# Kernel tuning notes

Measured on AMD Instinct MI355X. Metric: run time of the kernel, lower is better.

The kernel has to match this reference:

```python
import jax, jax.numpy as jnp
import numpy as np

N = 20000      # nodes (human PPI network scale)
E = 640000     # edges (avg degree 32)
PE, GOS, PROT = 128, 128, 480
OM_DIMS = [3, 3, 24, 24]          # transcriptome, proteome, effectome, interactome
D = 384                           # latent_space_dimension = 128 * 3 (jk 'cat')
H = 128                           # hidden_channels per layer
NEG_SLOPE = 0.1


def setup_inputs() -> dict:
    key = jax.random.key(0)
    ks = jax.random.split(key, 64)
    rn = lambda k, shp, s=0.05: jax.random.normal(k, shp, jnp.float32) * s
    inp = {
        "x": jax.random.normal(ks[0], (N, PE + GOS + PROT), jnp.float32),
        "x_ft": jax.random.normal(ks[1], (N, sum(OM_DIMS)), jnp.float32),
        "edge_index": jax.random.randint(ks[2], (2, E), 0, N),
    }
    i = 3
    def lin(fin, fout, name):
        nonlocal i
        inp["W_" + name] = rn(ks[i], (fin, fout)); inp["b_" + name] = jnp.zeros((fout,), jnp.float32)
        i += 1
    lin(PE, D, "pe"); lin(GOS, D, "gos"); lin(PROT, D, "prot")
    for j, d in enumerate(OM_DIMS):
        lin(d, D, f"om{j}")
    dims = [D, H, H, H]
    for j in range(3):
        lin(dims[j], dims[j + 1], f"c{j}")   # feature-branch GCN convs
        lin(dims[j], dims[j + 1], f"o{j}")   # omics-branch GCN convs
    lin(2 * D, D, "lat")
    lin(D, H, "drug"); lin(D, H, "dis")
    lin(H, 2, "odrug"); lin(H, 2, "odis")
    return inp


def _gcn(x, W, b, src, dst, deg_inv):
    # GCNConv(improved=True): A_hat = A + 2I, sym norm D^-1/2 A_hat D^-1/2
    h = x @ W                                  # [N, F_out]
    coef = deg_inv[src] * deg_inv[dst]         # [E]
    agg = jax.ops.segment_sum(h[src] * coef[:, None], dst, num_segments=N)
    agg = agg + h * (2.0 * deg_inv * deg_inv)[:, None]   # self loops (weight 2)
    return agg + b


def reference(x, x_ft, edge_index,
              W_pe, b_pe, W_gos, b_gos, W_prot, b_prot,
              W_om0, b_om0, W_om1, b_om1, W_om2, b_om2, W_om3, b_om3,
              W_c0, b_c0, W_o0, b_o0, W_c1, b_c1, W_o1, b_o1, W_c2, b_c2, W_o2, b_o2,
              W_lat, b_lat, W_drug, b_drug, W_dis, b_dis,
              W_odrug, b_odrug, W_odis, b_odis):
    act = lambda t: jax.nn.leaky_relu(t, NEG_SLOPE)
    src, dst = edge_index[0], edge_index[1]
    deg = jax.ops.segment_sum(jnp.ones((E,), jnp.float32), dst, num_segments=N) + 2.0
    deg_inv = jax.lax.rsqrt(deg)

    # encoders (features branch): pe | gosemsim | prot_emb slices of x
    pe = x[:, :PE]; gos = x[:, PE:PE + GOS]; prot = x[:, PE + GOS:PE + GOS + PROT]
    h = act(pe @ W_pe + b_pe + gos @ W_gos + b_gos + prot @ W_prot + b_prot)

    # encoders (omics branch): 3|3|24|24 slices of x_ft
    offs = np.cumsum([0] + OM_DIMS)
    Wom = [W_om0, W_om1, W_om2, W_om3]; bom = [b_om0, b_om1, b_om2, b_om3]
    g = act(sum(x_ft[:, offs[j]:offs[j + 1]] @ Wom[j] + bom[j] for j in range(4)))

    Wc = [W_c0, W_c1, W_c2]; bc = [b_c0, b_c1, b_c2]
    Wo = [W_o0, W_o1, W_o2]; bo = [b_o0, b_o1, b_o2]
    hs, gs = [], []
    for j in range(3):
        h = act(_gcn(h, Wc[j], bc[j], src, dst, deg_inv)); hs.append(h)
        g = act(_gcn(g, Wo[j], bo[j], src, dst, deg_inv)); gs.append(g)
    jk = jnp.concatenate(hs, axis=-1)          # [N, 384]
    jk_om = jnp.concatenate(gs, axis=-1)       # [N, 384]

    z = act(jnp.concatenate([jk, jk_om], axis=-1) @ W_lat + b_lat)  # [N, 384]
    drug = act(z @ W_drug + b_drug) @ W_odrug + b_odrug             # [N, 2]
    dis = act(z @ W_dis + b_dis) @ W_odis + b_odis                  # [N, 2]
    return jnp.concatenate([drug, dis], axis=-1)                    # [N, 4]
```

## Files before the change

### kernel.cpp

```cpp
#include <hip/hip_runtime.h>
#include <cstdint>

#define NN 20000
#define NNP 20096
#define NE 640000
#define NEG_SLOPE 0.1f
#define NSCAN 79
#define NSL 8
#define NPSL 2500
#define FBPS 160

typedef unsigned short ushort_t;
typedef __attribute__((ext_vector_type(8))) short short8;
typedef __attribute__((ext_vector_type(4))) float f32x4;
typedef __attribute__((ext_vector_type(2))) float f32x2;

__device__ __forceinline__ unsigned short f2bf(float f) {
    union { float f; unsigned u; } v; v.f = f;
    unsigned r = v.u + 0x7fffu + ((v.u >> 16) & 1u);
    return (unsigned short)(r >> 16);
}
__device__ __forceinline__ float bflo(unsigned u) { return __uint_as_float(u << 16); }
__device__ __forceinline__ float bfhi(unsigned u) { return __uint_as_float(u & 0xffff0000u); }

__device__ __forceinline__ int swz(int r) { return (r ^ (r >> 2)) & 3; }

__device__ __forceinline__ void gld_lds16(const void* g, void* l) {
    __builtin_amdgcn_global_load_lds(
        (const __attribute__((address_space(1))) void*)g,
        (__attribute__((address_space(3))) void*)l,
        16, 0, 0);
}

#define O_CAT   0
#define O_OM    282624
#define O_C0    307200
#define O_O0    356352
#define O_C1    405504
#define O_O1    421888
#define O_C2    438272
#define O_O2    454656
#define O_LAT   471040
#define O_HEADS 765952
#define WT_TOTAL 864256

__global__ __launch_bounds__(256) void pack_weights(
    const float* __restrict__ Wpe, const float* __restrict__ Wgos, const float* __restrict__ Wprot,
    const float* __restrict__ bpe, const float* __restrict__ bgos, const float* __restrict__ bprot,
    const float* __restrict__ Wom0, const float* __restrict__ Wom1,
    const float* __restrict__ Wom2, const float* __restrict__ Wom3,
    const float* __restrict__ bom0, const float* __restrict__ bom1,
    const float* __restrict__ bom2, const float* __restrict__ bom3,
    const float* __restrict__ Wc0, const float* __restrict__ Wo0,
    const float* __restrict__ Wc1, const float* __restrict__ Wo1,
    const float* __restrict__ Wc2, const float* __restrict__ Wo2,
    const float* __restrict__ Wlat,
    const float* __restrict__ Wdrug, const float* __restrict__ Wdis,
    const float* __restrict__ bdrug, const float* __restrict__ bdis,
    ushort_t* __restrict__ Wt, float* __restrict__ bcat, float* __restrict__ bomc,
    float* __restrict__ bheads)
{
    int i = blockIdx.x * blockDim.x + threadIdx.x;
    if (i < 282624) {
        int m = i / 736, k = i % 736;
        float v = (k < 128) ? Wpe[k * 384 + m]
                : (k < 256) ? Wgos[(k - 128) * 384 + m]
                            : Wprot[(k - 256) * 384 + m];
        Wt[O_CAT + i] = f2bf(v);
        return;
    }
    i -= 282624;
    if (i < 24576) {
        int m = i / 64, k = i % 64;
        float v = (k < 3)  ? Wom0[k * 384 + m]
                : (k < 6)  ? Wom1[(k - 3) * 384 + m]
                : (k < 30) ? Wom2[(k - 6) * 384 + m]
                : (k < 54) ? Wom3[(k - 30) * 384 + m] : 0.f;
        Wt[O_OM + i] = f2bf(v);
        return;
    }
    i -= 24576;
    if (i < 49152) { int m = i / 384, k = i % 384; Wt[O_C0 + i] = f2bf(Wc0[k * 128 + m]); return; }
    i -= 49152;
    if (i < 49152) { int m = i / 384, k = i % 384; Wt[O_O0 + i] = f2bf(Wo0[k * 128 + m]); return; }
    i -= 49152;
    if (i < 16384) { int m = i / 128, k = i % 128; Wt[O_C1 + i] = f2bf(Wc1[k * 128 + m]); return; }
    i -= 16384;
    if (i < 16384) { int m = i / 128, k = i % 128; Wt[O_O1 + i] = f2bf(Wo1[k * 128 + m]); return; }
    i -= 16384;
    if (i < 16384) { int m = i / 128, k = i % 128; Wt[O_C2 + i] = f2bf(Wc2[k * 128 + m]); return; }
    i -= 16384;
    if (i < 16384) { int m = i / 128, k = i % 128; Wt[O_O2 + i] = f2bf(Wo2[k * 128 + m]); return; }
    i -= 16384;
    if (i < 294912) { int m = i / 768, k = i % 768; Wt[O_LAT + i] = f2bf(Wlat[k * 384 + m]); return; }
    i -= 294912;
    if (i < 98304) {
        int m = i / 384, k = i % 384;
        float v = (m < 128) ? Wdrug[k * 128 + m] : Wdis[k * 128 + (m - 128)];
        Wt[O_HEADS + i] = f2bf(v);
        return;
    }
    i -= 98304;
    if (i < 384) { bcat[i] = bpe[i] + bgos[i] + bprot[i]; return; }
    i -= 384;
    if (i < 384) { bomc[i] = bom0[i] + bom1[i] + bom2[i] + bom3[i]; return; }
    i -= 384;
    if (i < 256) { bheads[i] = (i < 128) ? bdrug[i] : bdis[i - 128]; return; }
}

#define CVT_T1 (NN * 736 / 4)
__global__ __launch_bounds__(256) void convert_inputs(
    const float* __restrict__ x, const float* __restrict__ xft,
    ushort_t* __restrict__ xb, ushort_t* __restrict__ xftb)
{
    int i = blockIdx.x * blockDim.x + threadIdx.x;
    if (i < CVT_T1) {
        int base = i * 4;
        float4 v = *reinterpret_cast<const float4*>(&x[base]);
        unsigned long long p = (unsigned long long)f2bf(v.x)
                             | ((unsigned long long)f2bf(v.y) << 16)
                             | ((unsigned long long)f2bf(v.z) << 32)
                             | ((unsigned long long)f2bf(v.w) << 48);
        *reinterpret_cast<unsigned long long*>(&xb[base]) = p;
        return;
    }
    i -= CVT_T1;
    if (i < NN * 64) {
        int r = i >> 6, c = i & 63;
        float v = (c < 54) ? xft[r * 54 + c] : 0.f;
        xftb[i] = f2bf(v);
    }
}

__global__ __launch_bounds__(256) void count_deg_sliced(const int* __restrict__ dst, int* __restrict__ cnt)
{
    const int slice = blockIdx.x & (NSL - 1);
    const int blk = blockIdx.x >> 3;
    const int lo = slice * NPSL, hi = lo + NPSL;
    for (int e = blk * 256 + threadIdx.x; e < NE; e += FBPS * 256) {
        int d = dst[e];
        if (d >= lo && d < hi) atomicAdd(&cnt[d], 1);
    }
}

__global__ __launch_bounds__(256) void scan_blocksums(const int* __restrict__ cnt, int* __restrict__ bsum,
                                                      float* __restrict__ deg_inv)
{
    __shared__ int s[256];
    int t = threadIdx.x, i = blockIdx.x * 256 + t;
    int v = (i < NN) ? cnt[i] : 0;
    if (i < NN) deg_inv[i] = rsqrtf((float)v + 2.0f);
    s[t] = v;
    __syncthreads();
    for (int off = 128; off; off >>= 1) {
        if (t < off) s[t] += s[t + off];
        __syncthreads();
    }
    if (t == 0) bsum[blockIdx.x] = s[0];
}

__global__ __launch_bounds__(128) void scan_tops(const int* __restrict__ bsum,
                                                 int* __restrict__ boff, int* __restrict__ ofs)
{
    __shared__ int s[NSCAN];
    int t = threadIdx.x;
    if (t < NSCAN) s[t] = bsum[t];
    __syncthreads();
    if (t == 0) {
        int run = 0;
        for (int b = 0; b < NSCAN; b++) { int x = s[b]; s[b] = run; run += x; }
        ofs[NN] = run;
    }
    __syncthreads();
    if (t < NSCAN) boff[t] = s[t];
}

__global__ __launch_bounds__(256) void scan_apply(const int* __restrict__ cnt, const int* __restrict__ boff,
                                                  int* __restrict__ ofs, int* __restrict__ cursor)
{
    __shared__ int s[256];
    int t = threadIdx.x, i = blockIdx.x * 256 + t;
    int v = (i < NN) ? cnt[i] : 0;
    s[t] = v;
    __syncthreads();
    for (int off = 1; off < 256; off <<= 1) {
        int u = (t >= off) ? s[t - off] : 0;
        __syncthreads();
        s[t] += u;
        __syncthreads();
    }
    int excl = s[t] - v + boff[blockIdx.x];
    if (i < NN) { ofs[i] = excl; cursor[i] = excl; }
}

__global__ __launch_bounds__(256) void fill_csr_sliced(
    const int* __restrict__ src, const int* __restrict__ dst,
    const float* __restrict__ deg_inv, int* __restrict__ cursor,
    uint2* __restrict__ csr_pk)
{
    const int slice = blockIdx.x & (NSL - 1);
    const int blk = blockIdx.x >> 3;
    const int lo = slice * NPSL, hi = lo + NPSL;
    for (int e = blk * 256 + threadIdx.x; e < NE; e += FBPS * 256) {
        int d = dst[e];
        if (d >= lo && d < hi) {
            int s = src[e];
            int p = atomicAdd(&cursor[d], 1);
            float cf = deg_inv[s] * deg_inv[d];
            csr_pk[p] = make_uint2((unsigned)s * 256u, __float_as_uint(cf));
        }
    }
}

template<int BN, bool BIASACT, bool OUT_BF16>
__device__ __forceinline__ void gemm_body(
    ushort_t* As, ushort_t* Bs,
    const ushort_t* __restrict__ A, int lda,
    const ushort_t* __restrict__ Wt,
    const float* __restrict__ bias,
    float* __restrict__ Cf, ushort_t* __restrict__ Cb, int ldc,
    int nrows, int K, int row0, int col0)
{
    constexpr int BK = 32;
    constexpr int NI = (BN == 128) ? 4 : 2;

    const int t = threadIdx.x;
    const int w = t >> 6, lane = t & 63;
    const int wr = w >> 1, wc = w & 1;
    const int m16 = lane & 15, quad = lane >> 4;
    const int sr = lane >> 2;
    const int pgrp = lane & 3;

    f32x4 acc[4][NI];
#pragma unroll
    for (int mi = 0; mi < 4; mi++)
#pragma unroll
        for (int ni = 0; ni < NI; ni++) acc[mi][ni] = (f32x4)0.f;

    for (int k0 = 0; k0 < K; k0 += BK) {
#pragma unroll
        for (int p = 0; p < 2; p++) {
            int c = p * 4 + w;
            int r = c * 16 + sr;
            int q = pgrp ^ swz(r);
            gld_lds16(&A[(size_t)(row0 + r) * lda + k0 + q * 8], &As[c * 512]);
        }
#pragma unroll
        for (int p = 0; p < BN / 64; p++) {
            int c = p * 4 + w;
            int r = c * 16 + sr;
            int q = pgrp ^ swz(r);
            gld_lds16(&Wt[(size_t)(col0 + r) * K + k0 + q * 8], &Bs[c * 512]);
        }
        __syncthreads();

        short8 af[4], bfr[NI];
#pragma unroll
        for (int mi = 0; mi < 4; mi++) {
            int r = wr * 64 + mi * 16 + m16;
            int p = quad ^ swz(r);
            af[mi] = *reinterpret_cast<const short8*>(&As[r * 32 + p * 8]);
        }
#pragma unroll
        for (int ni = 0; ni < NI; ni++) {
            int n = wc * (NI * 16) + ni * 16 + m16;
            int p = quad ^ swz(n);
            bfr[ni] = *reinterpret_cast<const short8*>(&Bs[n * 32 + p * 8]);
        }
#pragma unroll
        for (int mi = 0; mi < 4; mi++)
#pragma unroll
            for (int ni = 0; ni < NI; ni++)
                acc[mi][ni] = __builtin_amdgcn_mfma_f32_16x16x32_bf16(af[mi], bfr[ni], acc[mi][ni], 0, 0, 0);
        __syncthreads();
    }

#pragma unroll
    for (int mi = 0; mi < 4; mi++) {
#pragma unroll
        for (int reg = 0; reg < 4; reg++) {
            int grow = row0 + wr * 64 + mi * 16 + quad * 4 + reg;
            if (grow >= nrows) continue;
#pragma unroll
            for (int ni = 0; ni < NI; ni++) {
                int gcol = col0 + wc * (NI * 16) + ni * 16 + m16;
                float v = acc[mi][ni][reg];
                if constexpr (BIASACT) {
                    v += bias[gcol];
                    v = (v > 0.f) ? v : NEG_SLOPE * v;
                }
                if constexpr (OUT_BF16) Cb[(size_t)grow * ldc + gcol] = f2bf(v);
                else                    Cf[(size_t)grow * ldc + gcol] = v;
            }
        }
    }
}

template<int BN, bool BIASACT, bool OUT_BF16>
__global__ __launch_bounds__(256) void mfma_gemm(
    const ushort_t* __restrict__ A, int lda,
    const ushort_t* __restrict__ Wt,
    const float* __restrict__ bias,
    float* __restrict__ Cf, ushort_t* __restrict__ Cb, int ldc,
    int nrows, int K)
{
    __shared__ ushort_t As[128 * 32];
    __shared__ ushort_t Bs[BN * 32];
    gemm_body<BN, BIASACT, OUT_BF16>(As, Bs, A, lda, Wt, bias, Cf, Cb, ldc, nrows, K,
                                     blockIdx.y * 128, blockIdx.x * BN);
}

__global__ __launch_bounds__(256) void mfma_gemm_dual(
    const ushort_t* __restrict__ A0, const ushort_t* __restrict__ A1, int lda,
    const ushort_t* __restrict__ W0, const ushort_t* __restrict__ W1,
    ushort_t* __restrict__ C0, ushort_t* __restrict__ C1, int ldc,
    int nrows, int K)
{
    __shared__ ushort_t As[128 * 32];
    __shared__ ushort_t Bs[64 * 32];
    const ushort_t* A  = blockIdx.z ? A1 : A0;
    const ushort_t* Wt = blockIdx.z ? W1 : W0;
    ushort_t*       Cb = blockIdx.z ? C1 : C0;
    gemm_body<64, false, true>(As, Bs, A, lda, Wt, nullptr, nullptr, Cb, ldc, nrows, K,
                               blockIdx.y * 128, blockIdx.x * 64);
}

__global__ __launch_bounds__(256) void aggregate_wave(
    const ushort_t* __restrict__ tabA, const ushort_t* __restrict__ tabB,
    const float* __restrict__ bc, const float* __restrict__ bo,
    const int* __restrict__ ofs, const uint2* __restrict__ csr_pk,
    const float* __restrict__ deg_inv,
    ushort_t* __restrict__ outb, int hcol, int gcol)
{
    __shared__ uint2 s_pk[4][64];
    const int w = threadIdx.x >> 6, lane = threadIdx.x & 63;
    const int task = blockIdx.x * 4 + w;
    const int slice = task / NN;
    const int i = task - slice * NN;
    const int chain = slice >> 1, half = slice & 1;
    const char* __restrict__ tabc = (const char*)(chain ? tabB : tabA);
    const float* __restrict__ bias = chain ? bo : bc;
    const int el = lane >> 3;
    const int fq = lane & 7;
    const unsigned lbyte = (unsigned)(half * 128 + fq * 16);

    const int start = ofs[i], end = ofs[i + 1];
    float acc[8];
#pragma unroll
    for (int q = 0; q < 8; q++) acc[q] = 0.f;

    for (int base = start; base < end; base += 64) {
        int n = end - base; if (n > 64) n = 64;
        if (lane < n) s_pk[w][lane] = csr_pk[base + lane];
        int j = el;
        for (; j + 8 < n; j += 16) {
            uint2 e0 = s_pk[w][j];
            uint2 e1 = s_pk[w][j + 8];
            uint4 p0 = *reinterpret_cast<const uint4*>(tabc + (e0.x + lbyte));
            uint4 p1 = *reinterpret_cast<const uint4*>(tabc + (e1.x + lbyte));
            float c0 = __uint_as_float(e0.y), c1 = __uint_as_float(e1.y);
            acc[0] = fmaf(bflo(p0.x), c0, acc[0]); acc[1] = fmaf(bfhi(p0.x), c0, acc[1]);
            acc[2] = fmaf(bflo(p0.y), c0, acc[2]); acc[3] = fmaf(bfhi(p0.y), c0, acc[3]);
            acc[4] = fmaf(bflo(p0.z), c0, acc[4]); acc[5] = fmaf(bfhi(p0.z), c0, acc[5]);
            acc[6] = fmaf(bflo(p0.w), c0, acc[6]); acc[7] = fmaf(bfhi(p0.w), c0, acc[7]);
            acc[0] = fmaf(bflo(p1.x), c1, acc[0]); acc[1] = fmaf(bfhi(p1.x), c1, acc[1]);
            acc[2] = fmaf(bflo(p1.y), c1, acc[2]); acc[3] = fmaf(bfhi(p1.y), c1, acc[3]);
            acc[4] = fmaf(bflo(p1.z), c1, acc[4]); acc[5] = fmaf(bfhi(p1.z), c1, acc[5]);
            acc[6] = fmaf(bflo(p1.w), c1, acc[6]); acc[7] = fmaf(bfhi(p1.w), c1, acc[7]);
        }
        if (j < n) {
            uint2 e0 = s_pk[w][j];
            uint4 p0 = *reinterpret_cast<const uint4*>(tabc + (e0.x + lbyte));
            float c0 = __uint_as_float(e0.y);
            acc[0] = fmaf(bflo(p0.x), c0, acc[0]); acc[1] = fmaf(bfhi(p0.x), c0, acc[1]);
            acc[2] = fmaf(bflo(p0.y), c0, acc[2]); acc[3] = fmaf(bfhi(p0.y), c0, acc[3]);
            acc[4] = fmaf(bflo(p0.z), c0, acc[4]); acc[5] = fmaf(bfhi(p0.z), c0, acc[5]);
            acc[6] = fmaf(bflo(p0.w), c0, acc[6]); acc[7] = fmaf(bfhi(p0.w), c0, acc[7]);
        }
    }
#pragma unroll
    for (int m = 8; m <= 32; m <<= 1) {
#pragma unroll
        for (int q = 0; q < 8; q++) acc[q] += __shfl_xor(acc[q], m);
    }
    if (el == 0) {
        float di = deg_inv[i];
        float c = 2.f * di * di;
        uint4 pv = *reinterpret_cast<const uint4*>(tabc + ((unsigned)i * 256u + lbyte));
        float sv[8] = {bflo(pv.x), bfhi(pv.x), bflo(pv.y), bfhi(pv.y),
                       bflo(pv.z), bfhi(pv.z), bflo(pv.w), bfhi(pv.w)};
        const int coloff = half * 64 + fq * 8;
        uint4 o;
        unsigned* op = &o.x;
#pragma unroll
        for (int q = 0; q < 8; q += 2) {
            float v0 = fmaf(sv[q],     c, acc[q])     + bias[coloff + q];
            float v1 = fmaf(sv[q + 1], c, acc[q + 1]) + bias[coloff + q + 1];
            v0 = (v0 > 0.f) ? v0 : NEG_SLOPE * v0;
            v1 = (v1 > 0.f) ? v1 : NEG_SLOPE * v1;
            op[q >> 1] = (unsigned)f2bf(v0) | ((unsigned)f2bf(v1) << 16);
        }
        int col = (chain ? gcol : hcol) + coloff;
        *reinterpret_cast<uint4*>(&outb[(size_t)i * 768 + col]) = o;
    }
}

__global__ __launch_bounds__(256) void heads_kernel(
    const float* __restrict__ tmpH,
    const float* __restrict__ Wod, const float* __restrict__ bod,
    const float* __restrict__ Wos, const float* __restrict__ bos,
    float* __restrict__ out)
{
    int w = threadIdx.x >> 6, lane = threadIdx.x & 63;
    int i = blockIdx.x * 4 + w;
    if (i >= NN) return;
    float a0 = 0.f, a1 = 0.f, d0 = 0.f, d1 = 0.f;
#pragma unroll
    for (int p = 0; p < 2; p++) {
        int k = lane + p * 64;
        float vd = tmpH[(size_t)i * 256 + k];
        float vs = tmpH[(size_t)i * 256 + 128 + k];
        a0 = fmaf(vd, Wod[k * 2 + 0], a0);
        a1 = fmaf(vd, Wod[k * 2 + 1], a1);
        d0 = fmaf(vs, Wos[k * 2 + 0], d0);
        d1 = fmaf(vs, Wos[k * 2 + 1], d1);
    }
    for (int off = 32; off; off >>= 1) {
        a0 += __shfl_down(a0, off);
        a1 += __shfl_down(a1, off);
        d0 += __shfl_down(d0, off);
        d1 += __shfl_down(d1, off);
    }
    if (lane == 0) {
        out[(size_t)i * 4 + 0] = a0 + bod[0];
        out[(size_t)i * 4 + 1] = a1 + bod[1];
        out[(size_t)i * 4 + 2] = d0 + bos[0];
        out[(size_t)i * 4 + 3] = d1 + bos[1];
    }
}

extern "C" void kernel_launch(void* const* d_in, const int* in_sizes, int n_in,
                              void* d_out, int out_size, void* d_ws, size_t ws_size,
                              hipStream_t stream)
{
    const float* x      = (const float*)d_in[0];
    const float* x_ft   = (const float*)d_in[1];
    const int*   eidx   = (const int*)d_in[2];
    const float* W_pe   = (const float*)d_in[3];
    const float* b_pe   = (const float*)d_in[4];
    const float* W_gos  = (const float*)d_in[5];
    const float* b_gos  = (const float*)d_in[6];
    const float* W_prot = (const float*)d_in[7];
    const float* b_prot = (const float*)d_in[8];
    const float* W_om0  = (const float*)d_in[9];
    const float* b_om0  = (const float*)d_in[10];
    const float* W_om1  = (const float*)d_in[11];
    const float* b_om1  = (const float*)d_in[12];
    const float* W_om2  = (const float*)d_in[13];
    const float* b_om2  = (const float*)d_in[14];
    const float* W_om3  = (const float*)d_in[15];
    const float* b_om3  = (const float*)d_in[16];
    const float* W_c[3] = {(const float*)d_in[17], (const float*)d_in[21], (const float*)d_in[25]};
    const float* b_c[3] = {(const float*)d_in[18], (const float*)d_in[22], (const float*)d_in[26]};
    const float* W_o[3] = {(const float*)d_in[19], (const float*)d_in[23], (const float*)d_in[27]};
    const float* b_o[3] = {(const float*)d_in[20], (const float*)d_in[24], (const float*)d_in[28]};
    const float* W_lat  = (const float*)d_in[29];
    const float* b_lat  = (const float*)d_in[30];
    const float* W_drug = (const float*)d_in[31];
    const float* b_drug = (const float*)d_in[32];
    const float* W_dis  = (const float*)d_in[33];
    const float* b_dis  = (const float*)d_in[34];
    const float* W_odrug= (const float*)d_in[35];
    const float* b_odrug= (const float*)d_in[36];
    const float* W_odis = (const float*)d_in[37];
    const float* b_odis = (const float*)d_in[38];
    float* out = (float*)d_out;

    const int* e_src = eidx;
    const int* e_dst = eidx + NE;

    char* p = (char*)d_ws;
    auto alloc = [&](size_t bytes) -> void* {
        void* r = (void*)p;
        p += (bytes + 255) & ~(size_t)255;
        return r;
    };
    ushort_t* Wt    = (ushort_t*)alloc((size_t)WT_TOTAL * 2);
    float* bcat     = (float*)alloc(384 * 4);
    float* bomc     = (float*)alloc(384 * 4);
    float* bheads   = (float*)alloc(256 * 4);
    float* deg_inv  = (float*)alloc((size_t)NN * 4);
    int*   cnt      = (int*)alloc((size_t)NN * 4);
    int*   ofs      = (int*)alloc((size_t)(NN + 1) * 4);
    int*   cursor   = (int*)alloc((size_t)NN * 4);
    int*   bsum     = (int*)alloc((size_t)NSCAN * 4);
    int*   boff     = (int*)alloc((size_t)NSCAN * 4);
    uint2* csr_pk   = (uint2*)alloc((size_t)NE * 8);
    ushort_t* xb    = (ushort_t*)alloc((size_t)NNP * 736 * 2);
    ushort_t* xftb  = (ushort_t*)alloc((size_t)NNP * 64 * 2);
    ushort_t* h0b   = (ushort_t*)alloc((size_t)NNP * 384 * 2);
    ushort_t* g0b   = (ushort_t*)alloc((size_t)NNP * 384 * 2);
    ushort_t* jkb   = (ushort_t*)alloc((size_t)NNP * 768 * 2);
    ushort_t* zb    = (ushort_t*)alloc((size_t)NNP * 384 * 2);
    ushort_t* tmpAb = (ushort_t*)alloc((size_t)NNP * 128 * 2);
    ushort_t* tmpBb = (ushort_t*)alloc((size_t)NNP * 128 * 2);
    float* tmpH     = (float*)alloc((size_t)NNP * 256 * 4);
    (void)ws_size; (void)in_sizes; (void)n_in; (void)out_size;

    {
        int total = WT_TOTAL + 384 + 384 + 256;
        pack_weights<<<dim3((total + 255) / 256), dim3(256), 0, stream>>>(
            W_pe, W_gos, W_prot, b_pe, b_gos, b_prot,
            W_om0, W_om1, W_om2, W_om3, b_om0, b_om1, b_om2, b_om3,
            W_c[0], W_o[0], W_c[1], W_o[1], W_c[2], W_o[2],
            W_lat, W_drug, W_dis, b_drug, b_dis, Wt, bcat, bomc, bheads);
    }
    convert_inputs<<<dim3((CVT_T1 + NN * 64 + 255) / 256), dim3(256), 0, stream>>>(x, x_ft, xb, xftb);

    hipMemsetAsync(cnt, 0, (size_t)NN * 4, stream);
    count_deg_sliced<<<dim3(NSL * FBPS), dim3(256), 0, stream>>>(e_dst, cnt);
    scan_blocksums<<<dim3(NSCAN), dim3(256), 0, stream>>>(cnt, bsum, deg_inv);
    scan_tops<<<dim3(1), dim3(128), 0, stream>>>(bsum, boff, ofs);
    scan_apply<<<dim3(NSCAN), dim3(256), 0, stream>>>(cnt, boff, ofs, cursor);
    fill_csr_sliced<<<dim3(NSL * FBPS), dim3(256), 0, stream>>>(e_src, e_dst, deg_inv, cursor, csr_pk);

    mfma_gemm<128, true, true><<<dim3(3, 157), dim3(256), 0, stream>>>(
        xb, 736, Wt + O_CAT, bcat, nullptr, h0b, 384, NN, 736);
    mfma_gemm<128, true, true><<<dim3(3, 157), dim3(256), 0, stream>>>(
        xftb, 64, Wt + O_OM, bomc, nullptr, g0b, 384, NN, 64);

    mfma_gemm_dual<<<dim3(2, 157, 2), dim3(256), 0, stream>>>(
        h0b, g0b, 384, Wt + O_C0, Wt + O_O0, tmpAb, tmpBb, 128, NN, 384);
    aggregate_wave<<<dim3(NN), dim3(256), 0, stream>>>(
        tmpAb, tmpBb, b_c[0], b_o[0], ofs, csr_pk, deg_inv, jkb, 0, 384);

    mfma_gemm_dual<<<dim3(2, 157, 2), dim3(256), 0, stream>>>(
        jkb + 0, jkb + 384, 768, Wt + O_C1, Wt + O_O1, tmpAb, tmpBb, 128, NN, 128);
    aggregate_wave<<<dim3(NN), dim3(256), 0, stream>>>(
        tmpAb, tmpBb, b_c[1], b_o[1], ofs, csr_pk, deg_inv, jkb, 128, 512);

    mfma_gemm_dual<<<dim3(2, 157, 2), dim3(256), 0, stream>>>(
        jkb + 128, jkb + 512, 768, Wt + O_C2, Wt + O_O2, tmpAb, tmpBb, 128, NN, 128);
    aggregate_wave<<<dim3(NN), dim3(256), 0, stream>>>(
        tmpAb, tmpBb, b_c[2], b_o[2], ofs, csr_pk, deg_inv, jkb, 256, 640);

    mfma_gemm<128, true, true><<<dim3(3, 157), dim3(256), 0, stream>>>(
        jkb, 768, Wt + O_LAT, b_lat, nullptr, zb, 384, NN, 768);

    mfma_gemm<128, true, false><<<dim3(2, 157), dim3(256), 0, stream>>>(
        zb, 384, Wt + O_HEADS, bheads, tmpH, nullptr, 256, NN, 384);
    heads_kernel<<<dim3((NN + 3) / 4), dim3(256), 0, stream>>>(
        tmpH, W_odrug, b_odrug, W_odis, b_odis, out);
}
```

Before: 499.8 us.

## Process both GCN chains per wave in fused aggregation, reading CSR directly

The aggregation kernel previously gave each wave one node-chain-half slice: 8 lanes per edge each loaded 16 bytes, and the 8 partial sums were then combined with shuffles. Now each wave handles one node across both chains and all 128 columns. 32 lanes cover the full 256-byte rows of both tables, and two edge groups are reduced with a single shuffle. This cuts repeated CSR reads and loop overhead fourfold and removes the LDS staging and the three-step shuffle reduction. In exchange, CSR entries are read directly from global memory by many lanes, and each wave has less edge-level parallelism.

```diff
diff --git a/kernel.cpp b/kernel.cpp
--- a/kernel.cpp
+++ b/kernel.cpp
@@ -325,71 +325,66 @@
                                blockIdx.y * 128, blockIdx.x * 64);
 }
 
-__global__ __launch_bounds__(256) void aggregate_wave(
+__global__ __launch_bounds__(256) void aggregate_fused(
     const ushort_t* __restrict__ tabA, const ushort_t* __restrict__ tabB,
     const float* __restrict__ bc, const float* __restrict__ bo,
     const int* __restrict__ ofs, const uint2* __restrict__ csr_pk,
     const float* __restrict__ deg_inv,
     ushort_t* __restrict__ outb, int hcol, int gcol)
 {
-    __shared__ uint2 s_pk[4][64];
     const int w = threadIdx.x >> 6, lane = threadIdx.x & 63;
-    const int task = blockIdx.x * 4 + w;
-    const int slice = task / NN;
-    const int i = task - slice * NN;
-    const int chain = slice >> 1, half = slice & 1;
-    const char* __restrict__ tabc = (const char*)(chain ? tabB : tabA);
-    const float* __restrict__ bias = chain ? bo : bc;
-    const int el = lane >> 3;
-    const int fq = lane & 7;
-    const unsigned lbyte = (unsigned)(half * 128 + fq * 16);
+    const int i = blockIdx.x * 4 + w;
+    const int el = lane >> 5;
+    const int fq = lane & 31;
+    const int chain = fq >> 4;
+    const unsigned lbyte = (unsigned)((fq & 15) * 16);
+    const char* __restrict__ tb = (const char*)(chain ? tabB : tabA);
 
     const int start = ofs[i], end = ofs[i + 1];
+    const float di = deg_inv[i];
+    const uint4 pv = *reinterpret_cast<const uint4*>(tb + ((unsigned)i * 256u + lbyte));
+
     float acc[8];
 #pragma unroll
     for (int q = 0; q < 8; q++) acc[q] = 0.f;
 
-    for (int base = start; base < end; base += 64) {
-        int n = end - base; if (n > 64) n = 64;
-        if (lane < n) s_pk[w][lane] = csr_pk[base + lane];
-        int j = el;
-        for (; j + 8 < n; j += 16) {
-            uint2 e0 = s_pk[w][j];
-            uint2 e1 = s_pk[w][j + 8];
-            uint4 p0 = *reinterpret_cast<const uint4*>(tabc + (e0.x + lbyte));
-            uint4 p1 = *reinterpret_cast<const uint4*>(tabc + (e1.x + lbyte));
-            float c0 = __uint_as_float(e0.y), c1 = __uint_as_float(e1.y);
-            acc[0] = fmaf(bflo(p0.x), c0, acc[0]); acc[1] = fmaf(bfhi(p0.x), c0, acc[1]);
-            acc[2] = fmaf(bflo(p0.y), c0, acc[2]); acc[3] = fmaf(bfhi(p0.y), c0, acc[3]);
-            acc[4] = fmaf(bflo(p0.z), c0, acc[4]); acc[5] = fmaf(bfhi(p0.z), c0, acc[5]);
-            acc[6] = fmaf(bflo(p0.w), c0, acc[6]); acc[7] = fmaf(bfhi(p0.w), c0, acc[7]);
-            acc[0] = fmaf(bflo(p1.x), c1, acc[0]); acc[1] = fmaf(bfhi(p1.x), c1, acc[1]);
-            acc[2] = fmaf(bflo(p1.y), c1, acc[2]); acc[3] = fmaf(bfhi(p1.y), c1, acc[3]);
-            acc[4] = fmaf(bflo(p1.z), c1, acc[4]); acc[5] = fmaf(bfhi(p1.z), c1, acc[5]);
-            acc[6] = fmaf(bflo(p1.w), c1, acc[6]); acc[7] = fmaf(bfhi(p1.w), c1, acc[7]);
-        }
-        if (j < n) {
-            uint2 e0 = s_pk[w][j];
-            uint4 p0 = *reinterpret_cast<const uint4*>(tabc + (e0.x + lbyte));
-            float c0 = __uint_as_float(e0.y);
-            acc[0] = fmaf(bflo(p0.x), c0, acc[0]); acc[1] = fmaf(bfhi(p0.x), c0, acc[1]);
-            acc[2] = fmaf(bflo(p0.y), c0, acc[2]); acc[3] = fmaf(bfhi(p0.y), c0, acc[3]);
-            acc[4] = fmaf(bflo(p0.z), c0, acc[4]); acc[5] = fmaf(bfhi(p0.z), c0, acc[5]);
-            acc[6] = fmaf(bflo(p0.w), c0, acc[6]); acc[7] = fmaf(bfhi(p0.w), c0, acc[7]);
-        }
-    }
-#pragma unroll
-    for (int m = 8; m <= 32; m <<= 1) {
-#pragma unroll
-        for (int q = 0; q < 8; q++) acc[q] += __shfl_xor(acc[q], m);
-    }
+#define FMA8(P, C) \
+    acc[0] = fmaf(bflo(P.x), C, acc[0]); acc[1] = fmaf(bfhi(P.x), C, acc[1]); \
+    acc[2] = fmaf(bflo(P.y), C, acc[2]); acc[3] = fmaf(bfhi(P.y), C, acc[3]); \
+    acc[4] = fmaf(bflo(P.z), C, acc[4]); acc[5] = fmaf(bfhi(P.z), C, acc[5]); \
+    acc[6] = fmaf(bflo(P.w), C, acc[6]); acc[7] = fmaf(bfhi(P.w), C, acc[7])
+
+    int j = start + el;
+    for (; j + 6 < end; j += 8) {
+        uint2 e0 = csr_pk[j];
+        uint2 e1 = csr_pk[j + 2];
+        uint2 e2 = csr_pk[j + 4];
+        uint2 e3 = csr_pk[j + 6];
+        uint4 p0 = *reinterpret_cast<const uint4*>(tb + (e0.x + lbyte));
+        uint4 p1 = *reinterpret_cast<const uint4*>(tb + (e1.x + lbyte));
+        uint4 p2 = *reinterpret_cast<const uint4*>(tb + (e2.x + lbyte));
+        uint4 p3 = *reinterpret_cast<const uint4*>(tb + (e3.x + lbyte));
+        float c0 = __uint_as_float(e0.y), c1 = __uint_as_float(e1.y);
+        float c2 = __uint_as_float(e2.y), c3 = __uint_as_float(e3.y);
+        FMA8(p0, c0); FMA8(p1, c1); FMA8(p2, c2); FMA8(p3, c3);
+    }
+    for (; j < end; j += 2) {
+        uint2 e0 = csr_pk[j];
+        uint4 p0 = *reinterpret_cast<const uint4*>(tb + (e0.x + lbyte));
+        float c0 = __uint_as_float(e0.y);
+        FMA8(p0, c0);
+    }
+#undef FMA8
+
+#pragma unroll
+    for (int q = 0; q < 8; q++) acc[q] += __shfl_xor(acc[q], 32);
+
     if (el == 0) {
-        float di = deg_inv[i];
-        float c = 2.f * di * di;
-        uint4 pv = *reinterpret_cast<const uint4*>(tabc + ((unsigned)i * 256u + lbyte));
+        const float* __restrict__ bias = chain ? bo : bc;
+        const int coloff = (fq & 15) * 8;
+        const float c = 2.f * di * di;
         float sv[8] = {bflo(pv.x), bfhi(pv.x), bflo(pv.y), bfhi(pv.y),
                        bflo(pv.z), bfhi(pv.z), bflo(pv.w), bfhi(pv.w)};
-        const int coloff = half * 64 + fq * 8;
         uint4 o;
         unsigned* op = &o.x;
 #pragma unroll
@@ -400,7 +395,7 @@
             v1 = (v1 > 0.f) ? v1 : NEG_SLOPE * v1;
             op[q >> 1] = (unsigned)f2bf(v0) | ((unsigned)f2bf(v1) << 16);
         }
-        int col = (chain ? gcol : hcol) + coloff;
+        const int col = (chain ? gcol : hcol) + coloff;
         *reinterpret_cast<uint4*>(&outb[(size_t)i * 768 + col]) = o;
     }
 }
@@ -531,17 +526,17 @@
 
     mfma_gemm_dual<<<dim3(2, 157, 2), dim3(256), 0, stream>>>(
         h0b, g0b, 384, Wt + O_C0, Wt + O_O0, tmpAb, tmpBb, 128, NN, 384);
-    aggregate_wave<<<dim3(NN), dim3(256), 0, stream>>>(
+    aggregate_fused<<<dim3(NN / 4), dim3(256), 0, stream>>>(
         tmpAb, tmpBb, b_c[0], b_o[0], ofs, csr_pk, deg_inv, jkb, 0, 384);
 
     mfma_gemm_dual<<<dim3(2, 157, 2), dim3(256), 0, stream>>>(
         jkb + 0, jkb + 384, 768, Wt + O_C1, Wt + O_O1, tmpAb, tmpBb, 128, NN, 128);
-    aggregate_wave<<<dim3(NN), dim3(256), 0, stream>>>(
+    aggregate_fused<<<dim3(NN / 4), dim3(256), 0, stream>>>(
         tmpAb, tmpBb, b_c[1], b_o[1], ofs, csr_pk, deg_inv, jkb, 128, 512);
 
     mfma_gemm_dual<<<dim3(2, 157, 2), dim3(256), 0, stream>>>(
         jkb + 128, jkb + 512, 768, Wt + O_C2, Wt + O_O2, tmpAb, tmpBb, 128, NN, 128);
-    aggregate_wave<<<dim3(NN), dim3(256), 0, stream>>>(
+    aggregate_fused<<<dim3(NN / 4), dim3(256), 0, stream>>>(
         tmpAb, tmpBb, b_c[2], b_o[2], ofs, csr_pk, deg_inv, jkb, 256, 640);
 
     mfma_gemm<128, true, true><<<dim3(3, 157), dim3(256), 0, stream>>>(
```

After: 495.5 us. About the same (-0.9%).
